# Kernel tuning notes

Hardware: AMD Instinct MI355X
Metric: run time of the kernel (lower is better)

## Reference

```python
import jax, jax.numpy as jnp
import numpy as np

# module hyperparameters (init_kwargs)
WEIGHT = 2e-9
SIGMA_RGB = 0.15   # images in [0,1]; equals canonical 15/255
SIGMA_XY = 100.0
SCALE = 0.5

N, C, K, H, W = 4, 3, 21, 128, 128


def _nearest(x, oh, ow):
    """torch F.interpolate(mode='nearest'): src = floor(dst * in/out)."""
    h, w = x.shape[-2], x.shape[-1]
    iy = jnp.floor(jnp.arange(oh) * (h / oh)).astype(jnp.int32)
    ix = jnp.floor(jnp.arange(ow) * (w / ow)).astype(jnp.int32)
    return x[..., iy[:, None], ix[None, :]]


def _bilinear(x, oh, ow):
    """torch F.interpolate(mode='bilinear', align_corners=False)."""
    h, w = x.shape[-2], x.shape[-1]

    def coords(o, s):
        c = (jnp.arange(o, dtype=jnp.float32) + 0.5) * (s / o) - 0.5
        c = jnp.clip(c, 0.0, s - 1.0)
        c0 = jnp.floor(c).astype(jnp.int32)
        c1 = jnp.minimum(c0 + 1, s - 1)
        return c0, c1, c - c0

    y0, y1, wy = coords(oh, h)
    x0, x1, wx = coords(ow, w)
    wy = wy[:, None]
    wx = wx[None, :]
    v00 = x[..., y0[:, None], x0[None, :]]
    v01 = x[..., y0[:, None], x1[None, :]]
    v10 = x[..., y1[:, None], x0[None, :]]
    v11 = x[..., y1[:, None], x1[None, :]]
    top = v00 * (1.0 - wx) + v01 * wx
    bot = v10 * (1.0 - wx) + v11 * wx
    return top * (1.0 - wy) + bot * wy


def setup_inputs() -> dict:
    key = jax.random.key(0)
    k1, k2 = jax.random.split(key)
    images = jax.random.uniform(k1, (N, C, H, W), jnp.float32)
    segmentations = jax.random.uniform(k2, (N, K, H, W), jnp.float32)
    ROIs = jnp.ones((N, H, W), jnp.float32)
    return {"images": images, "segmentations": segmentations, "ROIs": ROIs}


def reference(images, segmentations, ROIs):
    oh, ow = int(H * SCALE), int(W * SCALE)
    img_s = _nearest(images, oh, ow)           # [N,3,oh,ow]
    seg_s = _bilinear(segmentations, oh, ow)   # [N,K,oh,ow]
    roi_s = _nearest(ROIs, oh, ow)             # [N,oh,ow]
    seg_m = seg_s * roi_s[:, None]             # seg * ROI (per class)
    sxy = SIGMA_XY * SCALE

    # exact dense Gaussian bilateral kernel that the permutohedral lattice
    # (bilateralfilter_batch) approximates: k(i,j) = exp(-|p_i-p_j|^2/(2 sxy^2)
    #                                                  -|I_i-I_j|^2/(2 srgb^2))
    yy, xx = jnp.meshgrid(jnp.arange(oh, dtype=jnp.float32),
                          jnp.arange(ow, dtype=jnp.float32), indexing="ij")
    pos = jnp.stack([xx, yy], 0) / sxy         # [2,oh,ow]

    def per_image(img, seg):
        feat = jnp.concatenate([pos, img / SIGMA_RGB], 0).reshape(5, -1).T  # [P,5]
        sq = jnp.sum(feat * feat, axis=-1)                                  # [P]
        d2 = jnp.maximum(sq[:, None] + sq[None, :] - 2.0 * (feat @ feat.T), 0.0)
        Wk = jnp.exp(-0.5 * d2)                                             # [P,P]
        s = seg.reshape(K, -1)                                              # [K,P]
        AS = s @ Wk                                                         # filtered seg
        return jnp.sum(s * AS)

    vals = jax.vmap(per_image)(img_s, seg_m)   # [N]
    loss = -(jnp.sum(vals)) / N                # densecrf_loss
    return WEIGHT * loss
```

## Files before the change

kernel.cpp:

```cpp
#include <hip/hip_runtime.h>

#define NIMG 4
#define CCH  3
#define KCH  21
#define HIN  128
#define WIN  128
#define OH   64
#define OW   64
#define PPX  (OH*OW)
#define NPIX (NIMG*PPX)

#define PRE2 1.20112241f

#define SEGW  24
#define FEATW 8

#define BLOCK  256
#define JCHUNK 256
#define IBLK   64

#define NSLOT  64

typedef _Float16 half_t;
typedef half_t half8  __attribute__((ext_vector_type(8)));
typedef float  f32x4v __attribute__((ext_vector_type(4)));

#define FEATH_OFF ((size_t)NPIX*SEGW*2)
#define SQF_OFF   (FEATH_OFF + (size_t)NPIX*FEATW*2)
#define SLOT_OFF  (SQF_OFF + (size_t)NPIX*4)

__global__ __launch_bounds__(BLOCK) void crf_prep(const float* __restrict__ img,
                                                  const float* __restrict__ seg,
                                                  const float* __restrict__ roi,
                                                  half_t* __restrict__ segH,
                                                  half_t* __restrict__ featH,
                                                  float* __restrict__ sqF,
                                                  float* __restrict__ slots) {
    int g  = blockIdx.x * BLOCK + threadIdx.x;
    int q  = g >> 14;
    int pl = g & (NPIX - 1);
    int n  = pl >> 12;
    int p  = pl & (PPX - 1);
    int y = p >> 6, x = p & 63;
    int y2 = 2 * y, x2 = 2 * x;

    if (q < SEGW) {
        float v = 0.0f;
        if (q < KCH) {
            const float* s0 = seg + (((size_t)n * KCH + q) * HIN + y2) * WIN + x2;
            float r = roi[((size_t)n * HIN + y2) * WIN + x2];
            v = 0.25f * (s0[0] + s0[1] + s0[WIN] + s0[WIN + 1]) * r;
        }
        segH[(size_t)pl * SEGW + q] = (half_t)v;
    } else if (q == 24) {
        float fx = (float)x * (PRE2 / 50.0f);
        float fy = (float)y * (PRE2 / 50.0f);
        const size_t ib = (((size_t)n * CCH) * HIN + y2) * WIN + x2;
        float fr = img[ib]                         * (PRE2 / 0.15f);
        float fg = img[ib + (size_t)HIN * WIN]     * (PRE2 / 0.15f);
        float fb = img[ib + 2 * (size_t)HIN * WIN] * (PRE2 / 0.15f);
        half_t h0 = (half_t)fx, h1 = (half_t)fy, h2 = (half_t)fr,
               h3 = (half_t)fg, h4 = (half_t)fb;
        half8 fh = {h0, h1, h2, h3, h4, (half_t)0, (half_t)0, (half_t)0};
        *(half8*)(featH + (size_t)pl * FEATW) = fh;
        float a0 = (float)h0, a1 = (float)h1, a2 = (float)h2,
              a3 = (float)h3, a4 = (float)h4;
        sqF[pl] = 0.5f * (a0 * a0 + a1 * a1 + a2 * a2 + a3 * a3 + a4 * a4);
    } else if (q == 25) {
        if (pl < NSLOT) slots[pl * 16] = 0.0f;
    }
}

__global__ __launch_bounds__(BLOCK, 8) void crf_main(const half_t* __restrict__ segH,
                                                     const half_t* __restrict__ featH,
                                                     const float* __restrict__ sqF,
                                                     float* __restrict__ slots) {
    const int bx = blockIdx.x;
    const int n  = blockIdx.y;

    int g = 0;
#pragma unroll
    for (int t = 1; t < 16; ++t) {
        int off = 64 * t - 2 * t * (t - 1);
        if (bx >= off) g = t;
    }
    int rem = bx - (64 * g - 2 * g * (g - 1));
    int c   = 16 - g;
    int iq  = (rem >= c) + (rem >= 2 * c) + (rem >= 3 * c);
    int I   = 4 * g + iq;
    int J   = g + (rem - iq * c);
    const bool diag = (J == (I >> 2));

    const half_t* segN  = segH  + (size_t)n * PPX * SEGW;
    const half_t* featN = featH + (size_t)n * PPX * FEATW;
    const float*  sqN   = sqF   + (size_t)n * PPX;

    __shared__ alignas(16) half_t segJ[JCHUNK * SEGW];
    __shared__ alignas(16) half_t featJ[JCHUNK * FEATW];
    __shared__ alignas(16) half_t zrow[8];
    __shared__ float hJ[JCHUNK];
    __shared__ float wsum[BLOCK / 64];

    const int tid  = threadIdx.x;
    const int lane = tid & 63, wv = tid >> 6;
    const int m = lane & 15, quad = lane >> 4;
    const int i0 = I * IBLK + wv * 16;
    const int j0 = J * JCHUNK;
    const int kq = (quad < 2) ? quad : 2;

    half8 hz = {};

    half8 aseg  = *(const half8*)(segN  + (size_t)(i0 + m) * SEGW + kq * 8);
    half8 afeat = *(const half8*)(featN + (size_t)(i0 + m) * FEATW);
    f32x4v hi   = *(const f32x4v*)(sqN + i0 + quad * 4);
    if (quad == 3) aseg  = hz;
    if (quad != 0) afeat = hz;
    f32x4v nh = -hi;

    {
        const f32x4v* gsrc = (const f32x4v*)(segN + (size_t)j0 * SEGW);
        f32x4v* ldst = (f32x4v*)segJ;
#pragma unroll
        for (int v = 0; v < 3; ++v) ldst[tid + v * BLOCK] = gsrc[tid + v * BLOCK];
        ((f32x4v*)featJ)[tid] = ((const f32x4v*)(featN + (size_t)j0 * FEATW))[tid];
        hJ[tid] = sqN[j0 + tid];
        if (tid < 8) zrow[tid] = (half_t)0;
    }
    __syncthreads();

    const half_t* bsp; int bstep;
    if (quad == 3) { bsp = zrow;                       bstep = 0; }
    else           { bsp = segJ + m * SEGW + quad * 8; bstep = 16 * SEGW; }
    const half_t* bfp; int fstep;
    if (quad == 0) { bfp = featJ + m * FEATW;          fstep = 16 * FEATW; }
    else           { bfp = zrow;                       fstep = 0; }

    float hcv[16];
#pragma unroll
    for (int jt = 0; jt < 16; ++jt) hcv[jt] = hJ[jt * 16 + m];

    float racc = 0.0f;
    const f32x4v zero4 = {0.0f, 0.0f, 0.0f, 0.0f};

#pragma unroll
    for (int jt = 0; jt < JCHUNK / 16; ++jt) {
        half8 bseg = *(const half8*)(bsp + jt * bstep);
        half8 bft  = *(const half8*)(bfp + jt * fstep);
        float hc = hcv[jt];

        f32x4v c4 = {nh[0] - hc, nh[1] - hc, nh[2] - hc, nh[3] - hc};
        f32x4v E  = __builtin_amdgcn_mfma_f32_16x16x32_f16(afeat, bft, c4, 0, 0, 0);
        f32x4v Gs = __builtin_amdgcn_mfma_f32_16x16x32_f16(aseg, bseg, zero4, 0, 0, 0);

        if (!diag) {
#pragma unroll
            for (int r = 0; r < 4; ++r)
                racc = fmaf(__builtin_amdgcn_exp2f(E[r]), Gs[r], racc);
        } else {
            const int jg = j0 + jt * 16 + m;
#pragma unroll
            for (int r = 0; r < 4; ++r) {
                int ig = i0 + quad * 4 + r;
                float sel = (jg > ig) ? 1.0f : ((jg == ig) ? 0.0f : -100000.0f);
                racc = fmaf(__builtin_amdgcn_exp2f(E[r] + sel), Gs[r], racc);
            }
        }
    }

#pragma unroll
    for (int off = 32; off > 0; off >>= 1) racc += __shfl_down(racc, off);
    if (lane == 0) wsum[wv] = racc;
    __syncthreads();
    if (tid == 0) {
        float s = wsum[0] + wsum[1] + wsum[2] + wsum[3];
        if (!diag) s *= 2.0f;
        int slot = (bx + 544 * n) & (NSLOT - 1);
        atomicAdd(&slots[slot * 16], s);
    }
}

__global__ __launch_bounds__(64) void crf_final(const float* __restrict__ slots,
                                                float* __restrict__ out) {
    int lane = threadIdx.x;
    float v = slots[lane * 16];
#pragma unroll
    for (int off = 32; off > 0; off >>= 1) v += __shfl_down(v, off);
    if (lane == 0) out[0] = v * (-5.0e-10f);
}

extern "C" void kernel_launch(void* const* d_in, const int* in_sizes, int n_in,
                              void* d_out, int out_size, void* d_ws, size_t ws_size,
                              hipStream_t stream) {
    const float* img = (const float*)d_in[0];
    const float* seg = (const float*)d_in[1];
    const float* roi = (const float*)d_in[2];
    float* out = (float*)d_out;

    char* wsb = (char*)d_ws;
    half_t* segH  = (half_t*)(wsb);
    half_t* featH = (half_t*)(wsb + FEATH_OFF);
    float*  sqF   = (float*)(wsb + SQF_OFF);
    float*  slots = (float*)(wsb + SLOT_OFF);

    crf_prep<<<(NPIX * 26) / BLOCK, BLOCK, 0, stream>>>(img, seg, roi,
                                                        segH, featH, sqF, slots);

    dim3 grid(544, NIMG);
    crf_main<<<grid, BLOCK, 0, stream>>>(segH, featH, sqF, slots);

    crf_final<<<1, 64, 0, stream>>>(slots, out);
}
```

Baseline: 75.72 us.

## Split each wave over two i-tiles and half the j-tiles, skipping lower-triangle diagonal work

Measured after the change: 74.53 us, median of 2. About the same (-1.6%).

```diff
diff --git a/kernel.cpp b/kernel.cpp
--- a/kernel.cpp
+++ b/kernel.cpp
@@ -104,69 +104,106 @@
     const int tid  = threadIdx.x;
     const int lane = tid & 63, wv = tid >> 6;
     const int m = lane & 15, quad = lane >> 4;
-    const int i0 = I * IBLK + wv * 16;
-    const int j0 = J * JCHUNK;
-    const int kq = (quad < 2) ? quad : 2;
+    const int ih  = wv >> 1;
+    const int jt0 = (wv & 1) * 8;
+    const int ib0 = I * 4 + ih * 2;
+    const int ib1 = ib0 + 1;
+    const int i00 = ib0 << 4;
+    const int i01 = i00 + 16;
+    const int Jt  = J << 4;
+    const int kq  = (quad < 2) ? quad : 2;
 
     half8 hz = {};
 
-    half8 aseg  = *(const half8*)(segN  + (size_t)(i0 + m) * SEGW + kq * 8);
-    half8 afeat = *(const half8*)(featN + (size_t)(i0 + m) * FEATW);
-    f32x4v hi   = *(const f32x4v*)(sqN + i0 + quad * 4);
-    if (quad == 3) aseg  = hz;
-    if (quad != 0) afeat = hz;
-    f32x4v nh = -hi;
+    half8 aseg0  = *(const half8*)(segN  + (size_t)(i00 + m) * SEGW + kq * 8);
+    half8 aseg1  = *(const half8*)(segN  + (size_t)(i01 + m) * SEGW + kq * 8);
+    half8 afeat0 = *(const half8*)(featN + (size_t)(i00 + m) * FEATW);
+    half8 afeat1 = *(const half8*)(featN + (size_t)(i01 + m) * FEATW);
+    f32x4v hi0   = *(const f32x4v*)(sqN + i00 + quad * 4);
+    f32x4v hi1   = *(const f32x4v*)(sqN + i01 + quad * 4);
+    if (quad == 3) { aseg0 = hz; aseg1 = hz; }
+    if (quad != 0) { afeat0 = hz; afeat1 = hz; }
+    f32x4v nh0 = -hi0, nh1 = -hi1;
 
     {
-        const f32x4v* gsrc = (const f32x4v*)(segN + (size_t)j0 * SEGW);
+        const f32x4v* gsrc = (const f32x4v*)(segN + (size_t)((size_t)Jt << 4) * SEGW);
         f32x4v* ldst = (f32x4v*)segJ;
 #pragma unroll
         for (int v = 0; v < 3; ++v) ldst[tid + v * BLOCK] = gsrc[tid + v * BLOCK];
-        ((f32x4v*)featJ)[tid] = ((const f32x4v*)(featN + (size_t)j0 * FEATW))[tid];
-        hJ[tid] = sqN[j0 + tid];
+        ((f32x4v*)featJ)[tid] = ((const f32x4v*)(featN + (size_t)((size_t)Jt << 4) * FEATW))[tid];
+        hJ[tid] = sqN[(Jt << 4) + tid];
         if (tid < 8) zrow[tid] = (half_t)0;
     }
     __syncthreads();
 
     const half_t* bsp; int bstep;
-    if (quad == 3) { bsp = zrow;                       bstep = 0; }
-    else           { bsp = segJ + m * SEGW + quad * 8; bstep = 16 * SEGW; }
+    if (quad == 3) { bsp = zrow;                                    bstep = 0; }
+    else           { bsp = segJ + (jt0 * 16 + m) * SEGW + quad * 8; bstep = 16 * SEGW; }
     const half_t* bfp; int fstep;
-    if (quad == 0) { bfp = featJ + m * FEATW;          fstep = 16 * FEATW; }
-    else           { bfp = zrow;                       fstep = 0; }
-
-    float hcv[16];
-#pragma unroll
-    for (int jt = 0; jt < 16; ++jt) hcv[jt] = hJ[jt * 16 + m];
-
-    float racc = 0.0f;
+    if (quad == 0) { bfp = featJ + (jt0 * 16 + m) * FEATW;          fstep = 16 * FEATW; }
+    else           { bfp = zrow;                                    fstep = 0; }
+
+    float hcv[8];
+#pragma unroll
+    for (int t = 0; t < 8; ++t) hcv[t] = hJ[(jt0 + t) * 16 + m];
+
+    float racc0 = 0.0f, racc1 = 0.0f;
     const f32x4v zero4 = {0.0f, 0.0f, 0.0f, 0.0f};
 
 #pragma unroll
-    for (int jt = 0; jt < JCHUNK / 16; ++jt) {
-        half8 bseg = *(const half8*)(bsp + jt * bstep);
-        half8 bft  = *(const half8*)(bfp + jt * fstep);
-        float hc = hcv[jt];
-
-        f32x4v c4 = {nh[0] - hc, nh[1] - hc, nh[2] - hc, nh[3] - hc};
-        f32x4v E  = __builtin_amdgcn_mfma_f32_16x16x32_f16(afeat, bft, c4, 0, 0, 0);
-        f32x4v Gs = __builtin_amdgcn_mfma_f32_16x16x32_f16(aseg, bseg, zero4, 0, 0, 0);
-
-        if (!diag) {
-#pragma unroll
-            for (int r = 0; r < 4; ++r)
-                racc = fmaf(__builtin_amdgcn_exp2f(E[r]), Gs[r], racc);
-        } else {
-            const int jg = j0 + jt * 16 + m;
-#pragma unroll
-            for (int r = 0; r < 4; ++r) {
-                int ig = i0 + quad * 4 + r;
-                float sel = (jg > ig) ? 1.0f : ((jg == ig) ? 0.0f : -100000.0f);
-                racc = fmaf(__builtin_amdgcn_exp2f(E[r] + sel), Gs[r], racc);
+    for (int t = 0; t < 8; ++t) {
+        half8 bseg = *(const half8*)(bsp + t * bstep);
+        half8 bft  = *(const half8*)(bfp + t * fstep);
+        const float hc = hcv[t];
+        const int jb = Jt + jt0 + t;
+        const int jg = (jb << 4) + m;
+
+        if (!diag || jb >= ib0) {
+            f32x4v c4 = {nh0[0] - hc, nh0[1] - hc, nh0[2] - hc, nh0[3] - hc};
+            f32x4v E  = __builtin_amdgcn_mfma_f32_16x16x32_f16(afeat0, bft, c4, 0, 0, 0);
+            f32x4v Gs = __builtin_amdgcn_mfma_f32_16x16x32_f16(aseg0, bseg, zero4, 0, 0, 0);
+            if (!diag) {
+#pragma unroll
+                for (int r = 0; r < 4; ++r)
+                    racc0 = fmaf(__builtin_amdgcn_exp2f(E[r]), Gs[r], racc0);
+            } else if (jb > ib0) {
+#pragma unroll
+                for (int r = 0; r < 4; ++r)
+                    racc0 = fmaf(__builtin_amdgcn_exp2f(E[r] + 1.0f), Gs[r], racc0);
+            } else {
+#pragma unroll
+                for (int r = 0; r < 4; ++r) {
+                    int ig = i00 + quad * 4 + r;
+                    float sel = (jg > ig) ? 1.0f : ((jg == ig) ? 0.0f : -100000.0f);
+                    racc0 = fmaf(__builtin_amdgcn_exp2f(E[r] + sel), Gs[r], racc0);
+                }
             }
         }
-    }
-
+
+        if (!diag || jb >= ib1) {
+            f32x4v c4 = {nh1[0] - hc, nh1[1] - hc, nh1[2] - hc, nh1[3] - hc};
+            f32x4v E  = __builtin_amdgcn_mfma_f32_16x16x32_f16(afeat1, bft, c4, 0, 0, 0);
+            f32x4v Gs = __builtin_amdgcn_mfma_f32_16x16x32_f16(aseg1, bseg, zero4, 0, 0, 0);
+            if (!diag) {
+#pragma unroll
+                for (int r = 0; r < 4; ++r)
+                    racc1 = fmaf(__builtin_amdgcn_exp2f(E[r]), Gs[r], racc1);
+            } else if (jb > ib1) {
+#pragma unroll
+                for (int r = 0; r < 4; ++r)
+                    racc1 = fmaf(__builtin_amdgcn_exp2f(E[r] + 1.0f), Gs[r], racc1);
+            } else {
+#pragma unroll
+                for (int r = 0; r < 4; ++r) {
+                    int ig = i01 + quad * 4 + r;
+                    float sel = (jg > ig) ? 1.0f : ((jg == ig) ? 0.0f : -100000.0f);
+                    racc1 = fmaf(__builtin_amdgcn_exp2f(E[r] + sel), Gs[r], racc1);
+                }
+            }
+        }
+    }
+
+    float racc = racc0 + racc1;
 #pragma unroll
     for (int off = 32; off > 0; off >>= 1) racc += __shfl_down(racc, off);
     if (lane == 0) wsum[wv] = racc;
```
